# Performance work log

Hardware: AMD Instinct MI355X
Metric: run time of the kernel (lower is better)

Reference implementation:

```python
import jax, jax.numpy as jnp
import numpy as np

N_BINS = 15


def setup_inputs() -> dict:
    key = jax.random.key(0)
    k1, k2 = jax.random.split(key)
    N, C = 1000000, 100
    probs = jax.random.normal(k1, (N, C), dtype=jnp.float32)  # logits (is_logit=True path)
    labels = jax.random.randint(k2, (N,), 0, C, dtype=jnp.int64)
    return {"probs": probs, "labels": labels}


def reference(probs, labels):
    # ECELoss.forward with is_logit=True
    p = jax.nn.softmax(probs, axis=-1)
    confidences = jnp.max(p, axis=1)                    # [N]
    predictions = jnp.argmax(p, axis=1)                 # [N]
    correct = (predictions == labels).astype(p.dtype)   # [N]

    # bin i holds conf in (boundaries[i], boundaries[i+1]] -- matches gt(lower) & le(upper)
    boundaries = jnp.linspace(0.0, 1.0, N_BINS + 1)
    bin_idx = jnp.clip(jnp.searchsorted(boundaries, confidences, side="left") - 1, 0, N_BINS - 1)

    sum_conf = jax.ops.segment_sum(confidences, bin_idx, num_segments=N_BINS)
    sum_corr = jax.ops.segment_sum(correct, bin_idx, num_segments=N_BINS)
    # sum_b |avg_conf_b - acc_b| * (n_b / N) == sum_b |sum_conf_b - sum_corr_b| / N
    # (empty bins contribute |0 - 0| = 0, matching the prop_in_bin > 0 guard)
    n = jnp.asarray(confidences.shape[0], dtype=p.dtype)
    ece = jnp.sum(jnp.abs(sum_conf - sum_corr)) / n
    return ece.reshape(1)
```

## Files before the change

### kernel.cpp

```cpp
#include <hip/hip_runtime.h>
#include <math.h>

#define C 100
#define NBINS 15

__global__ __launch_bounds__(256) void ece_pass1(
    const float* __restrict__ probs, const int* __restrict__ labels,
    float* __restrict__ partials, int N, int G) {
  __shared__ float sbin[2 * NBINS];
  if (threadIdx.x < 2 * NBINS) sbin[threadIdx.x] = 0.0f;
  __syncthreads();

  const int lane  = threadIdx.x & 31;
  const int group = threadIdx.x >> 5;
  const int gpb   = blockDim.x >> 5;
  const int stride = G * gpb;

  for (int row = blockIdx.x * gpb + group; row < N; row += stride) {
    const float4* rp = (const float4*)(probs + (size_t)row * C);
    float4 v;
    if (lane < 25) v = rp[lane];
    else           v = make_float4(-INFINITY, -INFINITY, -INFINITY, -INFINITY);

    float mv = v.x; int mi = 4 * lane;
    if (v.y > mv) { mv = v.y; mi = 4 * lane + 1; }
    if (v.z > mv) { mv = v.z; mi = 4 * lane + 2; }
    if (v.w > mv) { mv = v.w; mi = 4 * lane + 3; }
    if (lane >= 25) mi = 0x7fffffff;

    #pragma unroll
    for (int m = 16; m >= 1; m >>= 1) {
      float ov = __shfl_xor(mv, m);
      int   oi = __shfl_xor(mi, m);
      if (ov > mv || (ov == mv && oi < mi)) { mv = ov; mi = oi; }
    }

    float se = 0.0f;
    if (lane < 25)
      se = __expf(v.x - mv) + __expf(v.y - mv) + __expf(v.z - mv) + __expf(v.w - mv);
    #pragma unroll
    for (int m = 16; m >= 1; m >>= 1) se += __shfl_xor(se, m);

    if (lane == 0) {
      float conf = 1.0f / se;
      float corr = (labels[row] == mi) ? 1.0f : 0.0f;
      int cnt = 0;
      #pragma unroll
      for (int i = 0; i <= NBINS; ++i)
        cnt += (((float)i / (float)NBINS) < conf) ? 1 : 0;
      int bin = cnt - 1;
      bin = bin < 0 ? 0 : (bin > NBINS - 1 ? NBINS - 1 : bin);
      atomicAdd(&sbin[bin], conf);
      atomicAdd(&sbin[NBINS + bin], corr);
    }
  }

  __syncthreads();
  if (threadIdx.x < 2 * NBINS)
    partials[(size_t)threadIdx.x * G + blockIdx.x] = sbin[threadIdx.x];
}

__global__ __launch_bounds__(1024) void ece_pass2(
    const float* __restrict__ partials, float* __restrict__ out, int G, int N) {
  __shared__ double cols[32];
  const int lane = threadIdx.x & 31;
  const int grp  = threadIdx.x >> 5;
  double s = 0.0;
  if (grp < 2 * NBINS) {
    for (int g = lane; g < G; g += 32)
      s += (double)partials[(size_t)grp * G + g];
  }
  #pragma unroll
  for (int m = 16; m >= 1; m >>= 1) s += __shfl_xor(s, m);
  if (lane == 0) cols[grp] = s;
  __syncthreads();
  if (threadIdx.x == 0) {
    double e = 0.0;
    for (int b = 0; b < NBINS; ++b) e += fabs(cols[b] - cols[NBINS + b]);
    out[0] = (float)(e / (double)N);
  }
}

extern "C" void kernel_launch(void* const* d_in, const int* in_sizes, int n_in,
                              void* d_out, int out_size, void* d_ws, size_t ws_size,
                              hipStream_t stream) {
  const float* probs  = (const float*)d_in[0];
  const int*   labels = (const int*)d_in[1];
  float*       out    = (float*)d_out;
  float*       partials = (float*)d_ws;

  const int N = in_sizes[1];

  int G = 2048;
  size_t need = (size_t)2 * NBINS * G * sizeof(float);
  if (ws_size < need) {
    G = (int)(ws_size / ((size_t)2 * NBINS * sizeof(float)));
    if (G < 1) G = 1;
  }

  ece_pass1<<<G, 256, 0, stream>>>(probs, labels, partials, N, G);
  ece_pass2<<<1, 1024, 0, stream>>>(partials, out, G, N);
}
```

Baseline: 553.3 us.

## Process two rows per 32-lane group and prefetch the next pair

```diff
diff --git a/kernel.cpp b/kernel.cpp
--- a/kernel.cpp
+++ b/kernel.cpp
@@ -3,6 +3,7 @@
 
 #define C 100
 #define NBINS 15
+#define NEG4 make_float4(-INFINITY, -INFINITY, -INFINITY, -INFINITY)
 
 __global__ __launch_bounds__(256) void ece_pass1(
     const float* __restrict__ probs, const int* __restrict__ labels,
@@ -11,39 +12,75 @@
   if (threadIdx.x < 2 * NBINS) sbin[threadIdx.x] = 0.0f;
   __syncthreads();
 
-  const int lane  = threadIdx.x & 31;
-  const int group = threadIdx.x >> 5;
-  const int gpb   = blockDim.x >> 5;
+  const int lane   = threadIdx.x & 31;
+  const int group  = threadIdx.x >> 5;
+  const int gpb    = blockDim.x >> 5;
   const int stride = G * gpb;
+  const int nPairs = (N + 1) >> 1;
 
-  for (int row = blockIdx.x * gpb + group; row < N; row += stride) {
-    const float4* rp = (const float4*)(probs + (size_t)row * C);
-    float4 v;
-    if (lane < 25) v = rp[lane];
-    else           v = make_float4(-INFINITY, -INFINITY, -INFINITY, -INFINITY);
+  int p = blockIdx.x * gpb + group;
+  bool valid = p < nPairs;
 
-    float mv = v.x; int mi = 4 * lane;
-    if (v.y > mv) { mv = v.y; mi = 4 * lane + 1; }
-    if (v.z > mv) { mv = v.z; mi = 4 * lane + 2; }
-    if (v.w > mv) { mv = v.w; mi = 4 * lane + 3; }
-    if (lane >= 25) mi = 0x7fffffff;
+  float4 a0 = NEG4, a1 = NEG4;
+  int lab = -1;
+  if (valid) {
+    const float4* rp = (const float4*)(probs + (size_t)p * (2 * C));
+    if (lane < 25) {
+      a0 = rp[lane];
+      if ((2 * p + 1) < N) a1 = rp[lane + 25];
+    }
+    if (lane < 2 && (2 * p + lane) < N) lab = labels[2 * p + lane];
+  }
+
+  while (valid) {
+    const int  pn     = p + stride;
+    const bool nvalid = pn < nPairs;
+
+    float4 b0 = NEG4, b1 = NEG4;
+    int nlab = -1;
+    if (nvalid) {
+      const float4* rp = (const float4*)(probs + (size_t)pn * (2 * C));
+      if (lane < 25) {
+        b0 = rp[lane];
+        if ((2 * pn + 1) < N) b1 = rp[lane + 25];
+      }
+      if (lane < 2 && (2 * pn + lane) < N) nlab = labels[2 * pn + lane];
+    }
+
+    float mv0 = a0.x; int mi0 = 4 * lane;
+    if (a0.y > mv0) { mv0 = a0.y; mi0 = 4 * lane + 1; }
+    if (a0.z > mv0) { mv0 = a0.z; mi0 = 4 * lane + 2; }
+    if (a0.w > mv0) { mv0 = a0.w; mi0 = 4 * lane + 3; }
+    float mv1 = a1.x; int mi1 = 4 * lane;
+    if (a1.y > mv1) { mv1 = a1.y; mi1 = 4 * lane + 1; }
+    if (a1.z > mv1) { mv1 = a1.z; mi1 = 4 * lane + 2; }
+    if (a1.w > mv1) { mv1 = a1.w; mi1 = 4 * lane + 3; }
+    if (lane >= 25) { mi0 = 0x7fffffff; mi1 = 0x7fffffff; }
 
     #pragma unroll
     for (int m = 16; m >= 1; m >>= 1) {
-      float ov = __shfl_xor(mv, m);
-      int   oi = __shfl_xor(mi, m);
-      if (ov > mv || (ov == mv && oi < mi)) { mv = ov; mi = oi; }
+      float o0 = __shfl_xor(mv0, m); int i0 = __shfl_xor(mi0, m);
+      float o1 = __shfl_xor(mv1, m); int i1 = __shfl_xor(mi1, m);
+      if (o0 > mv0 || (o0 == mv0 && i0 < mi0)) { mv0 = o0; mi0 = i0; }
+      if (o1 > mv1 || (o1 == mv1 && i1 < mi1)) { mv1 = o1; mi1 = i1; }
     }
 
-    float se = 0.0f;
-    if (lane < 25)
-      se = __expf(v.x - mv) + __expf(v.y - mv) + __expf(v.z - mv) + __expf(v.w - mv);
+    float se0 = 0.0f, se1 = 0.0f;
+    if (lane < 25) {
+      se0 = __expf(a0.x - mv0) + __expf(a0.y - mv0) +
+            __expf(a0.z - mv0) + __expf(a0.w - mv0);
+      se1 = __expf(a1.x - mv1) + __expf(a1.y - mv1) +
+            __expf(a1.z - mv1) + __expf(a1.w - mv1);
+    }
     #pragma unroll
-    for (int m = 16; m >= 1; m >>= 1) se += __shfl_xor(se, m);
+    for (int m = 16; m >= 1; m >>= 1) {
+      se0 += __shfl_xor(se0, m);
+      se1 += __shfl_xor(se1, m);
+    }
 
-    if (lane == 0) {
-      float conf = 1.0f / se;
-      float corr = (labels[row] == mi) ? 1.0f : 0.0f;
+    if (lane < 2 && (2 * p + lane) < N) {
+      float conf = (lane == 0) ? (1.0f / se0) : (1.0f / se1);
+      int   pred = (lane == 0) ? mi0 : mi1;
       int cnt = 0;
       #pragma unroll
       for (int i = 0; i <= NBINS; ++i)
@@ -51,8 +88,10 @@
       int bin = cnt - 1;
       bin = bin < 0 ? 0 : (bin > NBINS - 1 ? NBINS - 1 : bin);
       atomicAdd(&sbin[bin], conf);
-      atomicAdd(&sbin[NBINS + bin], corr);
+      atomicAdd(&sbin[NBINS + bin], (pred == lab) ? 1.0f : 0.0f);
     }
+
+    a0 = b0; a1 = b1; lab = nlab; p = pn; valid = nvalid;
   }
 
   __syncthreads();
@@ -84,9 +123,9 @@
 extern "C" void kernel_launch(void* const* d_in, const int* in_sizes, int n_in,
                               void* d_out, int out_size, void* d_ws, size_t ws_size,
                               hipStream_t stream) {
-  const float* probs  = (const float*)d_in[0];
-  const int*   labels = (const int*)d_in[1];
-  float*       out    = (float*)d_out;
+  const float* probs    = (const float*)d_in[0];
+  const int*   labels   = (const int*)d_in[1];
+  float*       out      = (float*)d_out;
   float*       partials = (float*)d_ws;
 
   const int N = in_sizes[1];
```

Result: no change. 561.3 us (+1.4%).

## Stage 64-row tiles in LDS per wavefront and compute softmax one row per lane

Applied to the files above, without the earlier changes.

```diff
diff --git a/kernel.cpp b/kernel.cpp
--- a/kernel.cpp
+++ b/kernel.cpp
@@ -3,55 +3,82 @@
 
 #define C 100
 #define NBINS 15
+#define ROWS 64
+#define RSTRIDE 103
+#define WPB 2
+#define TPB (WPB * 64)
 
-__global__ __launch_bounds__(256) void ece_pass1(
+__global__ __launch_bounds__(TPB) void ece_pass1(
     const float* __restrict__ probs, const int* __restrict__ labels,
     float* __restrict__ partials, int N, int G) {
+  __shared__ float tile[WPB][ROWS * RSTRIDE];
   __shared__ float sbin[2 * NBINS];
   if (threadIdx.x < 2 * NBINS) sbin[threadIdx.x] = 0.0f;
   __syncthreads();
 
-  const int lane  = threadIdx.x & 31;
-  const int group = threadIdx.x >> 5;
-  const int gpb   = blockDim.x >> 5;
-  const int stride = G * gpb;
+  const int  lane   = threadIdx.x & 63;
+  const int  w      = threadIdx.x >> 6;
+  const int  gw     = blockIdx.x * WPB + w;
+  const int  numW   = G * WPB;
+  const int  nTiles = (N + ROWS - 1) / ROWS;
+  const long totalF4 = ((long)N * C) / 4;
+  float* my = tile[w];
 
-  for (int row = blockIdx.x * gpb + group; row < N; row += stride) {
-    const float4* rp = (const float4*)(probs + (size_t)row * C);
-    float4 v;
-    if (lane < 25) v = rp[lane];
-    else           v = make_float4(-INFINITY, -INFINITY, -INFINITY, -INFINITY);
+  for (int t = gw; t < nTiles; t += numW) {
+    {
+      const float4* src = (const float4*)probs;
+      const long tb = (long)t * (ROWS * C / 4);
+      int row = lane / 25, c4 = lane - 25 * (lane / 25);
+      #pragma unroll
+      for (int k = 0; k < 25; ++k) {
+        long q = tb + k * 64 + lane;
+        float4 v = (q < totalF4) ? src[q] : make_float4(0.f, 0.f, 0.f, 0.f);
+        float* d = &my[row * RSTRIDE + 4 * c4];
+        d[0] = v.x; d[1] = v.y; d[2] = v.z; d[3] = v.w;
+        row += 2; c4 += 14; if (c4 >= 25) { c4 -= 25; row += 1; }
+      }
+    }
+    __threadfence_block();
 
-    float mv = v.x; int mi = 4 * lane;
-    if (v.y > mv) { mv = v.y; mi = 4 * lane + 1; }
-    if (v.z > mv) { mv = v.z; mi = 4 * lane + 2; }
-    if (v.w > mv) { mv = v.w; mi = 4 * lane + 3; }
-    if (lane >= 25) mi = 0x7fffffff;
+    const int grow = t * ROWS + lane;
+    if (grow < N) {
+      const int lab = labels[grow];
+      const float* rp = &my[lane * RSTRIDE];
 
-    #pragma unroll
-    for (int m = 16; m >= 1; m >>= 1) {
-      float ov = __shfl_xor(mv, m);
-      int   oi = __shfl_xor(mi, m);
-      if (ov > mv || (ov == mv && oi < mi)) { mv = ov; mi = oi; }
-    }
+      float m0 = -INFINITY, m1 = -INFINITY, m2 = -INFINITY, m3 = -INFINITY;
+      int   i0 = 0, i1 = 1, i2 = 2, i3 = 3;
+      #pragma unroll
+      for (int i = 0; i < C; i += 4) {
+        float x0 = rp[i], x1 = rp[i + 1], x2 = rp[i + 2], x3 = rp[i + 3];
+        if (x0 > m0) { m0 = x0; i0 = i; }
+        if (x1 > m1) { m1 = x1; i1 = i + 1; }
+        if (x2 > m2) { m2 = x2; i2 = i + 2; }
+        if (x3 > m3) { m3 = x3; i3 = i + 3; }
+      }
+      float M = m0; int idx = i0;
+      if (m1 > M || (m1 == M && i1 < idx)) { M = m1; idx = i1; }
+      if (m2 > M || (m2 == M && i2 < idx)) { M = m2; idx = i2; }
+      if (m3 > M || (m3 == M && i3 < idx)) { M = m3; idx = i3; }
 
-    float se = 0.0f;
-    if (lane < 25)
-      se = __expf(v.x - mv) + __expf(v.y - mv) + __expf(v.z - mv) + __expf(v.w - mv);
-    #pragma unroll
-    for (int m = 16; m >= 1; m >>= 1) se += __shfl_xor(se, m);
+      float s0 = 0.f, s1 = 0.f, s2 = 0.f, s3 = 0.f;
+      #pragma unroll
+      for (int i = 0; i < C; i += 4) {
+        s0 += __expf(rp[i]     - M);
+        s1 += __expf(rp[i + 1] - M);
+        s2 += __expf(rp[i + 2] - M);
+        s3 += __expf(rp[i + 3] - M);
+      }
+      float conf = 1.0f / ((s0 + s1) + (s2 + s3));
 
-    if (lane == 0) {
-      float conf = 1.0f / se;
-      float corr = (labels[row] == mi) ? 1.0f : 0.0f;
       int cnt = 0;
       #pragma unroll
       for (int i = 0; i <= NBINS; ++i)
         cnt += (((float)i / (float)NBINS) < conf) ? 1 : 0;
       int bin = cnt - 1;
       bin = bin < 0 ? 0 : (bin > NBINS - 1 ? NBINS - 1 : bin);
+
       atomicAdd(&sbin[bin], conf);
-      atomicAdd(&sbin[NBINS + bin], corr);
+      atomicAdd(&sbin[NBINS + bin], (lab == idx) ? 1.0f : 0.0f);
     }
   }
 
@@ -84,20 +111,20 @@
 extern "C" void kernel_launch(void* const* d_in, const int* in_sizes, int n_in,
                               void* d_out, int out_size, void* d_ws, size_t ws_size,
                               hipStream_t stream) {
-  const float* probs  = (const float*)d_in[0];
-  const int*   labels = (const int*)d_in[1];
-  float*       out    = (float*)d_out;
+  const float* probs    = (const float*)d_in[0];
+  const int*   labels   = (const int*)d_in[1];
+  float*       out      = (float*)d_out;
   float*       partials = (float*)d_ws;
 
   const int N = in_sizes[1];
 
-  int G = 2048;
+  int G = 768;
   size_t need = (size_t)2 * NBINS * G * sizeof(float);
   if (ws_size < need) {
     G = (int)(ws_size / ((size_t)2 * NBINS * sizeof(float)));
     if (G < 1) G = 1;
   }
 
-  ece_pass1<<<G, 256, 0, stream>>>(probs, labels, partials, N, G);
+  ece_pass1<<<G, TPB, 0, stream>>>(probs, labels, partials, N, G);
   ece_pass2<<<1, 1024, 0, stream>>>(partials, out, G, N);
 }
```

New measurement: 599.3 us. 1.08x slower.

## Process each row with four lanes and DPP reductions instead of 32-lane shuffles

Applied to the files above, without the earlier changes.

```diff
diff --git a/kernel.cpp b/kernel.cpp
--- a/kernel.cpp
+++ b/kernel.cpp
@@ -3,6 +3,9 @@
 
 #define C 100
 #define NBINS 15
+
+#define DPPF(x, ctrl) __int_as_float(__builtin_amdgcn_mov_dpp(__float_as_int(x), (ctrl), 0xF, 0xF, 0))
+#define DPPI(x, ctrl) __builtin_amdgcn_mov_dpp((x), (ctrl), 0xF, 0xF, 0)
 
 __global__ __launch_bounds__(256) void ece_pass1(
     const float* __restrict__ probs, const int* __restrict__ labels,
@@ -11,39 +14,60 @@
   if (threadIdx.x < 2 * NBINS) sbin[threadIdx.x] = 0.0f;
   __syncthreads();
 
-  const int lane  = threadIdx.x & 31;
-  const int group = threadIdx.x >> 5;
-  const int gpb   = blockDim.x >> 5;
-  const int stride = G * gpb;
+  const int l   = threadIdx.x & 3;
+  const int qid = (blockIdx.x * 256 + threadIdx.x) >> 2;
+  const int Q   = G * 64;
 
-  for (int row = blockIdx.x * gpb + group; row < N; row += stride) {
+  for (int row = qid; row < N; row += Q) {
     const float4* rp = (const float4*)(probs + (size_t)row * C);
-    float4 v;
-    if (lane < 25) v = rp[lane];
-    else           v = make_float4(-INFINITY, -INFINITY, -INFINITY, -INFINITY);
+    float4 v[6];
+    #pragma unroll
+    for (int j = 0; j < 6; ++j) v[j] = rp[l + 4 * j];
+    float4 t = rp[24];
+    const int lab = labels[row];
 
-    float mv = v.x; int mi = 4 * lane;
-    if (v.y > mv) { mv = v.y; mi = 4 * lane + 1; }
-    if (v.z > mv) { mv = v.z; mi = 4 * lane + 2; }
-    if (v.w > mv) { mv = v.w; mi = 4 * lane + 3; }
-    if (lane >= 25) mi = 0x7fffffff;
+    float mv = -INFINITY; int mi = 0;
+    #pragma unroll
+    for (int j = 0; j < 6; ++j) {
+      const int b = 4 * l + 16 * j;
+      if (v[j].x > mv) { mv = v[j].x; mi = b; }
+      if (v[j].y > mv) { mv = v[j].y; mi = b + 1; }
+      if (v[j].z > mv) { mv = v[j].z; mi = b + 2; }
+      if (v[j].w > mv) { mv = v[j].w; mi = b + 3; }
+    }
+    if (l == 0) {
+      if (t.x > mv) { mv = t.x; mi = 96; }
+      if (t.y > mv) { mv = t.y; mi = 97; }
+      if (t.z > mv) { mv = t.z; mi = 98; }
+      if (t.w > mv) { mv = t.w; mi = 99; }
+    }
 
-    #pragma unroll
-    for (int m = 16; m >= 1; m >>= 1) {
-      float ov = __shfl_xor(mv, m);
-      int   oi = __shfl_xor(mi, m);
+    {
+      float ov = DPPF(mv, 0xB1); int oi = DPPI(mi, 0xB1);
+      if (ov > mv || (ov == mv && oi < mi)) { mv = ov; mi = oi; }
+    }
+    {
+      float ov = DPPF(mv, 0x4E); int oi = DPPI(mi, 0x4E);
       if (ov > mv || (ov == mv && oi < mi)) { mv = ov; mi = oi; }
     }
 
-    float se = 0.0f;
-    if (lane < 25)
-      se = __expf(v.x - mv) + __expf(v.y - mv) + __expf(v.z - mv) + __expf(v.w - mv);
+    float s0 = 0.f, s1 = 0.f, s2 = 0.f, s3 = 0.f;
     #pragma unroll
-    for (int m = 16; m >= 1; m >>= 1) se += __shfl_xor(se, m);
+    for (int j = 0; j < 6; ++j) {
+      s0 += __expf(v[j].x - mv);
+      s1 += __expf(v[j].y - mv);
+      s2 += __expf(v[j].z - mv);
+      s3 += __expf(v[j].w - mv);
+    }
+    float se = (s0 + s1) + (s2 + s3);
+    if (l == 0)
+      se += __expf(t.x - mv) + __expf(t.y - mv) +
+            __expf(t.z - mv) + __expf(t.w - mv);
+    se += DPPF(se, 0xB1);
+    se += DPPF(se, 0x4E);
 
-    if (lane == 0) {
+    if (l == 0) {
       float conf = 1.0f / se;
-      float corr = (labels[row] == mi) ? 1.0f : 0.0f;
       int cnt = 0;
       #pragma unroll
       for (int i = 0; i <= NBINS; ++i)
@@ -51,7 +75,7 @@
       int bin = cnt - 1;
       bin = bin < 0 ? 0 : (bin > NBINS - 1 ? NBINS - 1 : bin);
       atomicAdd(&sbin[bin], conf);
-      atomicAdd(&sbin[NBINS + bin], corr);
+      atomicAdd(&sbin[NBINS + bin], (lab == mi) ? 1.0f : 0.0f);
     }
   }
 
@@ -84,9 +108,9 @@
 extern "C" void kernel_launch(void* const* d_in, const int* in_sizes, int n_in,
                               void* d_out, int out_size, void* d_ws, size_t ws_size,
                               hipStream_t stream) {
-  const float* probs  = (const float*)d_in[0];
-  const int*   labels = (const int*)d_in[1];
-  float*       out    = (float*)d_out;
+  const float* probs    = (const float*)d_in[0];
+  const int*   labels   = (const int*)d_in[1];
+  float*       out      = (float*)d_out;
   float*       partials = (float*)d_ws;
 
   const int N = in_sizes[1];
```

Result: faster. 533.8 us (-3.5%).
